# Kernel optimization log

Hardware: AMD Instinct MI355X
Metric: run time of the kernel (lower is better)

The kernel has to match this reference:

```python
import jax, jax.numpy as jnp
import numpy as np
import math
from jax import lax

TAU = 2
SIGMA_D2 = (TAU / 1.5) ** 2
SIGMA_TH2 = math.radians(20.0) ** 2

_offs = range(-TAU, TAU + 1)
OFFSETS = np.array([(dz, dy, dx) for dz in _offs for dy in _offs for dx in _offs
                    if dz or dy or dx], dtype=np.int32)  # (124, 3)
W_DIST = np.exp(-(OFFSETS.astype(np.float64) ** 2).sum(1) / SIGMA_D2).astype(np.float32)


def setup_inputs() -> dict:
    key = jax.random.key(0)
    k1, k2 = jax.random.split(key)
    n_pred = jax.random.normal(k1, (2, 3, 64, 64, 64), dtype=jnp.float32)
    source_pred = jax.random.normal(k2, (2, 1, 64, 64, 64), dtype=jnp.float32)
    return {"n_pred": n_pred, "source_pred": source_pred}


def reference(n_pred, source_pred):
    B, C, D, H, W = n_pred.shape
    pad = TAU
    # F.normalize(p=2, dim=1, eps=1e-6): divide by max(norm, eps)
    norm = jnp.sqrt(jnp.sum(n_pred * n_pred, axis=1, keepdims=True))
    n = n_pred / jnp.maximum(norm, 1e-6)

    prob = jax.nn.sigmoid(source_pred)            # (B,1,D,H,W)
    central_mask = prob > 0.5                      # (B,1,D,H,W)

    spat = ((0, 0), (0, 0), (pad, pad), (pad, pad), (pad, pad))
    padded_n = jnp.pad(n, spat)                    # zero pad like F.pad value=0
    padded_p = jnp.pad(prob, spat)

    offsets = jnp.asarray(OFFSETS)                 # (124,3)
    w_dist = jnp.asarray(W_DIST, dtype=n.dtype)    # (124,)

    def body(carry, xs):
        off, wd = xs
        start_n = (0, 0, pad + off[0], pad + off[1], pad + off[2])
        shifted_n = lax.dynamic_slice(padded_n, start_n, (B, C, D, H, W))
        shifted_p = lax.dynamic_slice(padded_p, start_n, (B, 1, D, H, W))
        dot = jnp.clip(jnp.sum(n * shifted_n, axis=1), -1.0, 1.0)  # (B,D,H,W)
        theta2 = jnp.arccos(dot) ** 2
        w_theta = jnp.exp(-theta2 / SIGMA_TH2)
        m = (central_mask & (shifted_p > 0.5))[:, 0].astype(n.dtype)  # (B,D,H,W)
        total, count = carry
        total = total + wd * jnp.sum(w_theta * m)
        count = count + jnp.sum(m)
        return (total, count), None

    init = (jnp.zeros((), n.dtype), jnp.zeros((), n.dtype))
    (total, count), _ = lax.scan(body, init, (offsets, w_dist))
    # reduction='mean' over masked elements; 0 if no valid pairs
    return jnp.where(count == 0, jnp.zeros((), n.dtype), total / count)
```

## Files before the change

### kernel.cpp

```cpp
#include <hip/hip_runtime.h>
#include <math.h>

#define PD 68
#define PD2 (PD * PD)
#define PVOL (PD * PD * PD)
#define NBLK2 1024

#define KE (-16.4140429822f)


__global__ __launch_bounds__(256) void pad_normalize_kernel(
    const float* __restrict__ n_pred,
    const float* __restrict__ src,
    float4* __restrict__ q)
{
    int idx = blockIdx.x * 256 + threadIdx.x;
    if (idx >= 2 * PVOL) return;
    int b = idx / PVOL;
    int r = idx - b * PVOL;
    int z = r / PD2;
    int r2 = r - z * PD2;
    int y = r2 / PD;
    int x = r2 - y * PD;
    int gx = x - 2, gy = y - 2, gz = z - 2;
    float4 v = make_float4(0.f, 0.f, 0.f, 0.f);
    if ((unsigned)gx < 64u && (unsigned)gy < 64u && (unsigned)gz < 64u) {
        const size_t cs = 262144;
        size_t vox = ((size_t)gz * 64 + gy) * 64 + gx;
        size_t off = (size_t)b * 3 * cs + vox;
        float xx = n_pred[off];
        float yy = n_pred[off + cs];
        float zz = n_pred[off + 2 * cs];
        float inv = 1.0f / fmaxf(sqrtf(xx * xx + yy * yy + zz * zz), 1e-6f);
        float m = (src[(size_t)b * cs + vox] > 0.0f) ? 1.0f : 0.0f;
        v = make_float4(xx * inv, yy * inv, zz * inv, m);
    }
    q[idx] = v;
}


__global__ __launch_bounds__(256) void stencil_col2_kernel(
    const float4* __restrict__ q, float2* __restrict__ partials)
{
    int x = threadIdx.x & 63;
    int y = blockIdx.x * 4 + (threadIdx.x >> 6);
    int z0 = blockIdx.y * 2;
    int b = blockIdx.z;
    const float4* base =
        q + (size_t)b * PVOL + ((size_t)(z0 + 2) * PD + (y + 2)) * PD + (x + 2);

    float4 c0 = base[0];
    float4 c1 = base[PD2];

    float tot = 0.0f, cf = 0.0f;

    auto app = [&](const float4& c, const float4& nb, float coff) {
        float dot = fmaf(c.x, nb.x, fmaf(c.y, nb.y, c.z * nb.z));
        float u = 1.0f - dot;
        float p = fmaf(u, 1.8990885e-3f, 5.5803571e-3f);
        p = fmaf(u, p, 1.8750000e-2f);
        p = fmaf(u, p, 8.3333333e-2f);
        p = fmaf(u, p, 1.0f);
        float uh = u * p * p;
        float w = __expf(fmaf(KE, uh, coff));
        float g = nb.w * c.w;
        tot = fmaf(w, g, tot);
        cf += g;
    };

    if (c0.w + c1.w != 0.0f) {
#pragma unroll
        for (int dy = -2; dy <= 2; ++dy) {
#pragma unroll
            for (int dx = -2; dx <= 2; ++dx) {
                if (dy > 0 || (dy == 0 && dx > 0)) {
                    float4 nb = base[dy * PD + dx];
                    app(c0, nb, -0.5625f * (float)(dy * dy + dx * dx));
                }
            }
        }
#pragma unroll
        for (int k = 1; k <= 3; ++k) {
#pragma unroll
            for (int dy = -2; dy <= 2; ++dy) {
#pragma unroll
                for (int dx = -2; dx <= 2; ++dx) {
                    float4 nb = base[k * PD2 + dy * PD + dx];
                    const int d2 = dy * dy + dx * dx;
                    if (k <= 2)
                        app(c0, nb, -0.5625f * (float)(k * k + d2));
                    const int dz1 = k - 1;
                    if (dz1 == 0) {
                        if (dy > 0 || (dy == 0 && dx > 0))
                            app(c1, nb, -0.5625f * (float)d2);
                    } else {
                        app(c1, nb, -0.5625f * (float)(dz1 * dz1 + d2));
                    }
                }
            }
        }
    }

#pragma unroll
    for (int s = 32; s > 0; s >>= 1) {
        tot += __shfl_down(tot, s, 64);
        cf  += __shfl_down(cf, s, 64);
    }
    __shared__ float sd[4], sc[4];
    int wid = threadIdx.x >> 6, lane = threadIdx.x & 63;
    if (lane == 0) { sd[wid] = tot; sc[wid] = cf; }
    __syncthreads();
    if (threadIdx.x == 0) {
        int bid = ((int)blockIdx.z * gridDim.y + blockIdx.y) * gridDim.x
                  + blockIdx.x;
        partials[bid] = make_float2(sd[0] + sd[1] + sd[2] + sd[3],
                                    sc[0] + sc[1] + sc[2] + sc[3]);
    }
}

__global__ __launch_bounds__(256) void reduce_kernel(
    const float2* __restrict__ partials, float* __restrict__ out)
{
    double t = 0.0, c = 0.0;
    for (int i = threadIdx.x; i < NBLK2; i += 256) {
        float2 p = partials[i];
        t += (double)p.x;
        c += (double)p.y;
    }
#pragma unroll
    for (int s = 32; s > 0; s >>= 1) {
        t += __shfl_down(t, s, 64);
        c += __shfl_down(c, s, 64);
    }
    __shared__ double sd[4], sc[4];
    int wid = threadIdx.x >> 6, lane = threadIdx.x & 63;
    if (lane == 0) { sd[wid] = t; sc[wid] = c; }
    __syncthreads();
    if (threadIdx.x == 0) {
        double T = sd[0] + sd[1] + sd[2] + sd[3];
        double C = sc[0] + sc[1] + sc[2] + sc[3];
        out[0] = (C == 0.0) ? 0.0f : (float)(T / C);
    }
}


#define TILE 8
#define HALO 2
#define LDIM 12
#define LSZ  1728
#define NVOX 512

__global__ __launch_bounds__(256) void repulsion_fused_kernel(
    const float* __restrict__ n_pred, const float* __restrict__ src,
    double* __restrict__ acc)
{
    __shared__ float4 sn[LSZ];
    __shared__ float rd[4], rc[4];
    const int tx = blockIdx.x * TILE, ty = blockIdx.y * TILE;
    const int b = blockIdx.z >> 3, tz = (blockIdx.z & 7) * TILE;
    const size_t cs = 262144;
    const float* npb = n_pred + (size_t)b * 3 * cs;
    const float* spb = src + (size_t)b * cs;
    for (int i = threadIdx.x; i < LSZ; i += 256) {
        int lx = i % LDIM, t = i / LDIM, ly = t % LDIM, lz = t / LDIM;
        int gx = tx + lx - HALO, gy = ty + ly - HALO, gz = tz + lz - HALO;
        float4 v = make_float4(0.f, 0.f, 0.f, 0.f);
        if ((unsigned)gx < 64u && (unsigned)gy < 64u && (unsigned)gz < 64u) {
            size_t off = ((size_t)gz * 64 + gy) * 64 + gx;
            float xx = npb[off], yy = npb[cs + off], zz = npb[2 * cs + off];
            float inv = 1.0f / fmaxf(sqrtf(xx * xx + yy * yy + zz * zz), 1e-6f);
            float m = (spb[off] > 0.0f) ? 1.0f : 0.0f;
            v = make_float4(xx * inv, yy * inv, zz * inv, m);
        }
        sn[i] = v;
    }
    __syncthreads();
    float tot = 0.0f, cf = 0.0f;
    for (int v = threadIdx.x; v < NVOX; v += 256) {
        int lx = (v & 7) + HALO, ly = ((v >> 3) & 7) + HALO, lz = (v >> 6) + HALO;
        int ci = (lz * LDIM + ly) * LDIM + lx;
        float4 c = sn[ci];
        if (c.w == 0.0f) continue;
#pragma unroll
        for (int dz = -2; dz <= 2; ++dz)
#pragma unroll
            for (int dy = -2; dy <= 2; ++dy)
#pragma unroll
                for (int dx = -2; dx <= 2; ++dx) {
                    if (dz == 0 && dy == 0 && dx == 0) continue;
                    const float coff =
                        -0.5625f * (float)(dz * dz + dy * dy + dx * dx);
                    float4 nb = sn[ci + (dz * LDIM + dy) * LDIM + dx];
                    float dot = fmaf(c.x, nb.x, fmaf(c.y, nb.y, c.z * nb.z));
                    float u = 1.0f - dot;
                    float p = fmaf(u, 1.8990885e-3f, 5.5803571e-3f);
                    p = fmaf(u, p, 1.8750000e-2f);
                    p = fmaf(u, p, 8.3333333e-2f);
                    p = fmaf(u, p, 1.0f);
                    float uh = u * p * p;
                    float w = __expf(fmaf(KE, uh, coff));
                    tot = fmaf(w, nb.w, tot);
                    cf += nb.w;
                }
    }
#pragma unroll
    for (int s = 32; s > 0; s >>= 1) {
        tot += __shfl_down(tot, s, 64);
        cf  += __shfl_down(cf, s, 64);
    }
    int wid = threadIdx.x >> 6, lane = threadIdx.x & 63;
    if (lane == 0) { rd[wid] = tot; rc[wid] = cf; }
    __syncthreads();
    if (threadIdx.x == 0) {
        atomicAdd(&acc[0], (double)rd[0] + rd[1] + rd[2] + rd[3]);
        atomicAdd(&acc[1], (double)rc[0] + rc[1] + rc[2] + rc[3]);
    }
}

__global__ void zero_acc_kernel(double* acc) { acc[0] = 0.0; acc[1] = 0.0; }

__global__ void finalize_kernel(const double* acc, float* out) {
    out[0] = (acc[1] == 0.0) ? 0.0f : (float)(acc[0] / acc[1]);
}


extern "C" void kernel_launch(void* const* d_in, const int* in_sizes, int n_in,
                              void* d_out, int out_size, void* d_ws, size_t ws_size,
                              hipStream_t stream) {
    const float* n_pred = (const float*)d_in[0];
    const float* src    = (const float*)d_in[1];

    const size_t vol_bytes = (size_t)2 * PVOL * sizeof(float4);
    const size_t need = vol_bytes + (size_t)NBLK2 * sizeof(float2);

    if (ws_size >= need) {
        float4* q = (float4*)d_ws;
        float2* partials = (float2*)((char*)d_ws + vol_bytes);
        int nblk = (2 * PVOL + 255) / 256;
        pad_normalize_kernel<<<nblk, 256, 0, stream>>>(n_pred, src, q);
        dim3 grid(16, 32, 2);
        stencil_col2_kernel<<<grid, 256, 0, stream>>>(q, partials);
        reduce_kernel<<<1, 256, 0, stream>>>(partials, (float*)d_out);
    } else {
        double* acc = (double*)d_ws;
        zero_acc_kernel<<<1, 1, 0, stream>>>(acc);
        dim3 grid(8, 8, 16);
        repulsion_fused_kernel<<<grid, 256, 0, stream>>>(n_pred, src, acc);
        finalize_kernel<<<1, 1, 0, stream>>>(acc, (float*)d_out);
    }
}
```

Before: 30.38 us.

## Store padded normals as fp16 with mask folded into vector norm

The padded normal volume is stored as half-precision 4-vectors instead of float4, with masked-out voxels zeroed so the mask is recovered from the squared norm. Dot products use the packed fp16 dot2 instruction with fp32 accumulation. Separate accumulators for the two center voxels are scaled by their recovered masks at the end. The aim is to halve the bytes written and re-read by the stencil and cut ALU work per neighbour. The cost is fp16 rounding error in the normals and the angle term, plus extra dot2 work to recompute each neighbour's norm.

New measurement: 35.32 us. +16.2%, slower.

```diff
diff --git a/kernel.cpp b/kernel.cpp
--- a/kernel.cpp
+++ b/kernel.cpp
@@ -1,5 +1,8 @@
 #include <hip/hip_runtime.h>
 #include <math.h>
+
+typedef _Float16 h2 __attribute__((ext_vector_type(2)));
+typedef _Float16 h4 __attribute__((ext_vector_type(4)));
 
 #define PD 68
 #define PD2 (PD * PD)
@@ -8,11 +11,19 @@
 
 #define KE (-16.4140429822f)
 
+__device__ __forceinline__ float hdot(h2 a, h2 b, float c) {
+#if __has_builtin(__builtin_amdgcn_fdot2)
+    return __builtin_amdgcn_fdot2(a, b, c, false);
+#else
+    return fmaf((float)a.x, (float)b.x, fmaf((float)a.y, (float)b.y, c));
+#endif
+}
+
 
 __global__ __launch_bounds__(256) void pad_normalize_kernel(
     const float* __restrict__ n_pred,
     const float* __restrict__ src,
-    float4* __restrict__ q)
+    h4* __restrict__ q)
 {
     int idx = blockIdx.x * 256 + threadIdx.x;
     if (idx >= 2 * PVOL) return;
@@ -23,7 +34,7 @@
     int y = r2 / PD;
     int x = r2 - y * PD;
     int gx = x - 2, gy = y - 2, gz = z - 2;
-    float4 v = make_float4(0.f, 0.f, 0.f, 0.f);
+    float vx = 0.f, vy = 0.f, vz = 0.f;
     if ((unsigned)gx < 64u && (unsigned)gy < 64u && (unsigned)gz < 64u) {
         const size_t cs = 262144;
         size_t vox = ((size_t)gz * 64 + gy) * 64 + gx;
@@ -32,30 +43,39 @@
         float yy = n_pred[off + cs];
         float zz = n_pred[off + 2 * cs];
         float inv = 1.0f / fmaxf(sqrtf(xx * xx + yy * yy + zz * zz), 1e-6f);
-        float m = (src[(size_t)b * cs + vox] > 0.0f) ? 1.0f : 0.0f;
-        v = make_float4(xx * inv, yy * inv, zz * inv, m);
-    }
-    q[idx] = v;
+        if (src[(size_t)b * cs + vox] > 0.0f) {
+            vx = xx * inv; vy = yy * inv; vz = zz * inv;
+        }
+    }
+    h4 h;
+    h.x = (_Float16)vx; h.y = (_Float16)vy; h.z = (_Float16)vz;
+    h.w = (_Float16)0.f;
+    q[idx] = h;
 }
 
 
 __global__ __launch_bounds__(256) void stencil_col2_kernel(
-    const float4* __restrict__ q, float2* __restrict__ partials)
+    const h4* __restrict__ q, float2* __restrict__ partials)
 {
     int x = threadIdx.x & 63;
     int y = blockIdx.x * 4 + (threadIdx.x >> 6);
     int z0 = blockIdx.y * 2;
     int b = blockIdx.z;
-    const float4* base =
+    const h4* base =
         q + (size_t)b * PVOL + ((size_t)(z0 + 2) * PD + (y + 2)) * PD + (x + 2);
 
-    float4 c0 = base[0];
-    float4 c1 = base[PD2];
-
-    float tot = 0.0f, cf = 0.0f;
-
-    auto app = [&](const float4& c, const float4& nb, float coff) {
-        float dot = fmaf(c.x, nb.x, fmaf(c.y, nb.y, c.z * nb.z));
+    h4 c0v = base[0];
+    h4 c1v = base[PD2];
+    h2 c0lo = {c0v.x, c0v.y}, c0hi = {c0v.z, c0v.w};
+    h2 c1lo = {c1v.x, c1v.y}, c1hi = {c1v.z, c1v.w};
+    float nnc0 = hdot(c0lo, c0lo, hdot(c0hi, c0hi, 0.f));
+    float nnc1 = hdot(c1lo, c1lo, hdot(c1hi, c1hi, 0.f));
+
+    float tot0 = 0.f, cf0 = 0.f, tot1 = 0.f, cf1 = 0.f;
+
+    auto app = [&](h2 clo, h2 chi, h2 lo, h2 hi, float nn, float coff,
+                   float& tt, float& cc) {
+        float dot = hdot(clo, lo, hdot(chi, hi, 0.f));
         float u = 1.0f - dot;
         float p = fmaf(u, 1.8990885e-3f, 5.5803571e-3f);
         p = fmaf(u, p, 1.8750000e-2f);
@@ -63,19 +83,21 @@
         p = fmaf(u, p, 1.0f);
         float uh = u * p * p;
         float w = __expf(fmaf(KE, uh, coff));
-        float g = nb.w * c.w;
-        tot = fmaf(w, g, tot);
-        cf += g;
+        tt = fmaf(w, nn, tt);
+        cc += nn;
     };
 
-    if (c0.w + c1.w != 0.0f) {
+    if (nnc0 + nnc1 > 0.5f) {
 #pragma unroll
         for (int dy = -2; dy <= 2; ++dy) {
 #pragma unroll
             for (int dx = -2; dx <= 2; ++dx) {
                 if (dy > 0 || (dy == 0 && dx > 0)) {
-                    float4 nb = base[dy * PD + dx];
-                    app(c0, nb, -0.5625f * (float)(dy * dy + dx * dx));
+                    h4 v = base[dy * PD + dx];
+                    h2 lo = {v.x, v.y}, hi = {v.z, v.w};
+                    float nn = hdot(lo, lo, hdot(hi, hi, 0.f));
+                    app(c0lo, c0hi, lo, hi, nn,
+                        -0.5625f * (float)(dy * dy + dx * dx), tot0, cf0);
                 }
             }
         }
@@ -85,21 +107,29 @@
             for (int dy = -2; dy <= 2; ++dy) {
 #pragma unroll
                 for (int dx = -2; dx <= 2; ++dx) {
-                    float4 nb = base[k * PD2 + dy * PD + dx];
+                    h4 v = base[k * PD2 + dy * PD + dx];
+                    h2 lo = {v.x, v.y}, hi = {v.z, v.w};
+                    float nn = hdot(lo, lo, hdot(hi, hi, 0.f));
                     const int d2 = dy * dy + dx * dx;
                     if (k <= 2)
-                        app(c0, nb, -0.5625f * (float)(k * k + d2));
+                        app(c0lo, c0hi, lo, hi, nn,
+                            -0.5625f * (float)(k * k + d2), tot0, cf0);
                     const int dz1 = k - 1;
                     if (dz1 == 0) {
                         if (dy > 0 || (dy == 0 && dx > 0))
-                            app(c1, nb, -0.5625f * (float)d2);
+                            app(c1lo, c1hi, lo, hi, nn,
+                                -0.5625f * (float)d2, tot1, cf1);
                     } else {
-                        app(c1, nb, -0.5625f * (float)(dz1 * dz1 + d2));
+                        app(c1lo, c1hi, lo, hi, nn,
+                            -0.5625f * (float)(dz1 * dz1 + d2), tot1, cf1);
                     }
                 }
             }
         }
     }
+
+    float tot = fmaf(tot0, nnc0, tot1 * nnc1);
+    float cf  = fmaf(cf0,  nnc0, cf1  * nnc1);
 
 #pragma unroll
     for (int s = 32; s > 0; s >>= 1) {
@@ -230,11 +260,11 @@
     const float* n_pred = (const float*)d_in[0];
     const float* src    = (const float*)d_in[1];
 
-    const size_t vol_bytes = (size_t)2 * PVOL * sizeof(float4);
+    const size_t vol_bytes = (size_t)2 * PVOL * sizeof(h4);
     const size_t need = vol_bytes + (size_t)NBLK2 * sizeof(float2);
 
     if (ws_size >= need) {
-        float4* q = (float4*)d_ws;
+        h4* q = (h4*)d_ws;
         float2* partials = (float2*)((char*)d_ws + vol_bytes);
         int nblk = (2 * PVOL + 255) / 256;
         pad_normalize_kernel<<<nblk, 256, 0, stream>>>(n_pred, src, q);
```
